# Kernel optimization log

Measured on AMD Instinct MI355X. Metric: run time of the kernel, lower is better.

## Reference

```python
import jax, jax.numpy as jnp
import numpy as np
import math

BATCH, NODES, IN_DIM = 8, 2048, 64
HEADS, OUT_DIM = 4, 32
D = HEADS * OUT_DIM
N_NEIGHBORS = 32


def setup_inputs() -> dict:
    key = jax.random.key(0)
    ks = jax.random.split(key, 6)
    s = lambda fan: 1.0 / np.sqrt(fan)
    return {
        "x": jax.random.normal(ks[0], (BATCH, NODES, IN_DIM), jnp.float32),
        "Wq": jax.random.normal(ks[1], (D, IN_DIM), jnp.float32) * s(IN_DIM),
        "bq": jnp.zeros((D,), jnp.float32),
        "Wk": jax.random.normal(ks[2], (D, IN_DIM), jnp.float32) * s(IN_DIM),
        "bk": jnp.zeros((D,), jnp.float32),
        "mlp_w": jax.random.normal(ks[3], (HEADS, HEADS), jnp.float32) * s(HEADS),
        "mlp_b": jnp.zeros((HEADS,), jnp.float32),
        "ln_g": jnp.ones((NODES,), jnp.float32),
        "ln_b": jnp.zeros((NODES,), jnp.float32),
    }


def _layernorm(x, g, b, eps=1e-5):
    m = x.mean(-1, keepdims=True)
    v = x.var(-1, keepdims=True)
    return (x - m) * jax.lax.rsqrt(v + eps) * g + b


def _forward(x, Wq, bq, Wk, bk, mlp_w, mlp_b, ln_g, ln_b):
    B, N, _ = x.shape
    # static graph branch (computed in the original forward, but its result is
    # never used in the returned adjacency -- kept for fidelity; DCE'd under jit)
    adj_static = jax.nn.softmax(
        jax.nn.relu(_layernorm(jnp.einsum('bnc,bmc->bnm', x, x), ln_g, ln_b)), axis=1)
    del adj_static

    q = x @ Wq.T + bq  # (B,N,D)
    k = x @ Wk.T + bk
    # (B,D,N) -> (B,H,d,N)
    q = q.transpose(0, 2, 1).reshape(B, HEADS, OUT_DIM, N)
    k = k.transpose(0, 2, 1).reshape(B, HEADS, OUT_DIM, N)
    q = q.transpose(0, 1, 3, 2)  # (B,H,N,d)

    # torch.split(query, chunk, dim=-1) splits q over out_dim, k over nodes; zip
    # truncates to the shorter list -> only min(nq,nk) chunks are processed.
    chunk = math.ceil(N / 2)
    nq = math.ceil(OUT_DIM / chunk)
    nk = math.ceil(N / chunk)
    inv_sqrt_d = jnp.float32(1.0 / math.sqrt(OUT_DIM))
    outs = []
    for i in range(min(nq, nk)):
        qc = q[..., i * chunk:(i + 1) * chunk]          # (B,H,N,dc)
        kc = k[..., i * chunk:(i + 1) * chunk]          # (B,H,d,Uc)
        a = jnp.einsum('bhnd,bhdu->bhnu', qc, kc) * inv_sqrt_d
        # dropout is identity in eval mode; soft-threshold with beta=0
        a = jnp.sign(a) * jax.nn.relu(jnp.abs(a))
        # 1x1 conv over head channels + relu, residual add
        a = jax.nn.relu(jnp.einsum('oh,bhnu->bonu', mlp_w, a)
                        + mlp_b[None, :, None, None]) + a
        outs.append(a)
    attn = jnp.concatenate(outs, axis=-1)               # (B,H,N,U)

    scores = attn.sum(axis=1)                           # (B,N,U)
    vals, idx = jax.lax.top_k(scores, N_NEIGHBORS)      # sorted, largest
    adj = jnp.zeros((B, N, N), x.dtype)
    bi = jnp.arange(B)[:, None, None]
    ni = jnp.arange(N)[None, :, None]
    return adj.at[bi, ni, idx].add(vals)


def reference(x, Wq, bq, Wk, bk, mlp_w, mlp_b, ln_g, ln_b):
    return _forward(x, Wq, bq, Wk, bk, mlp_w, mlp_b, ln_g, ln_b)
```

## Files before the change

kernel.cpp:

```cpp
#include <hip/hip_runtime.h>
#include <cstdint>
#include <cstddef>

#define BATCH 8
#define NODES 2048
#define IN_DIM 64
#define DTOT 128
#define NKEY 1024
#define QGROUPS 128
#define KGROUPS 64
#define SROW 1028

typedef _Float16 half8v __attribute__((ext_vector_type(8)));
typedef float float4v __attribute__((ext_vector_type(4)));
typedef float float2v __attribute__((ext_vector_type(2)));

__device__ __forceinline__ unsigned long long make_key(float v, int idx) {
    unsigned u = __float_as_uint(v);
    u = (u & 0x80000000u) ? ~u : (u | 0x80000000u);
    return ((unsigned long long)u << 32) | (unsigned)(1023 - idx);
}

__device__ __forceinline__ float key_val(unsigned hi) {
    return __uint_as_float((hi & 0x80000000u) ? (hi & 0x7fffffffu) : ~hi);
}

__global__ __launch_bounds__(256) void proj_qk(
    const float* __restrict__ x, const float* __restrict__ Wq, const float* __restrict__ bq,
    const float* __restrict__ Wk, const float* __restrict__ bk,
    _Float16* __restrict__ qfh, _Float16* __restrict__ qfl,
    _Float16* __restrict__ kfh, _Float16* __restrict__ kfl)
{
    __shared__ float xs[64 * 68];
    __shared__ float wsh[64 * 68];

    const int t = threadIdx.x;
    const int blk = blockIdx.x;
    const int b = blk / 96;
    const int idx = blk - b * 96;

    const float* W; const float* bias;
    _Float16* oh; _Float16* ol;
    int nbase, cbase; size_t gbase;
    float scale;
    if (idx < 64) {
        int nt = idx >> 1, ct = idx & 1;
        nbase = nt * 64; cbase = ct * 64;
        W = Wq; bias = bq; oh = qfh; ol = qfl;
        gbase = (size_t)b * QGROUPS + (nbase >> 4);
        scale = 0.17677669529663687f;
    } else {
        int i2 = idx - 64;
        int nt = i2 >> 1, ct = i2 & 1;
        nbase = nt * 64; cbase = ct * 64;
        W = Wk; bias = bk; oh = kfh; ol = kfl;
        gbase = (size_t)b * KGROUPS + (nbase >> 4);
        scale = 1.0f;
    }
    const int hbase = cbase >> 5;

    #pragma unroll
    for (int rep = 0; rep < 4; ++rep) {
        int f = rep * 256 + t;
        int r = f >> 4, d4 = f & 15;
        float4 xv = *(const float4*)(x + ((size_t)(b * NODES + nbase + r)) * IN_DIM + d4 * 4);
        *(float4*)(xs + r * 68 + d4 * 4) = xv;
        float4 wv = *(const float4*)(W + (size_t)(cbase + r) * IN_DIM + d4 * 4);
        *(float4*)(wsh + r * 68 + d4 * 4) = wv;
    }
    __syncthreads();

    const int w = t >> 6, l = t & 63;
    const int n_sel = w * 4 + (l >> 4);
    const int ul = l & 15;

    float acc[4][4];
    #pragma unroll
    for (int i = 0; i < 4; ++i)
        #pragma unroll
        for (int j = 0; j < 4; ++j) acc[i][j] = 0.f;

    #pragma unroll
    for (int d4 = 0; d4 < 16; ++d4) {
        float4 xv[4], wv[4];
        #pragma unroll
        for (int i = 0; i < 4; ++i)
            xv[i] = *(const float4*)(xs + (n_sel * 4 + i) * 68 + d4 * 4);
        #pragma unroll
        for (int j = 0; j < 4; ++j)
            wv[j] = *(const float4*)(wsh + (j * 16 + ul) * 68 + d4 * 4);
        #pragma unroll
        for (int i = 0; i < 4; ++i)
            #pragma unroll
            for (int j = 0; j < 4; ++j)
                acc[i][j] += xv[i].x * wv[j].x + xv[i].y * wv[j].y +
                             xv[i].z * wv[j].z + xv[i].w * wv[j].w;
    }
    __syncthreads();

    #pragma unroll
    for (int j = 0; j < 4; ++j) {
        float bv = bias[cbase + j * 16 + ul];
        #pragma unroll
        for (int i = 0; i < 4; ++i)
            xs[(n_sel * 4 + i) * 68 + j * 16 + ul] = (acc[i][j] + bv) * scale;
    }
    __syncthreads();

    #pragma unroll
    for (int rep = 0; rep < 2; ++rep) {
        int u = rep * 256 + t;
        int g = u >> 7, hh = (u >> 6) & 1, lf = u & 63;
        const float* src = xs + (g * 16 + (lf & 15)) * 68 + hh * 32 + (lf >> 4) * 8;
        float4 f0 = *(const float4*)src;
        float4 f1 = *(const float4*)(src + 4);
        float tmp[8] = {f0.x, f0.y, f0.z, f0.w, f1.x, f1.y, f1.z, f1.w};
        half8v hv, lv;
        #pragma unroll
        for (int e = 0; e < 8; ++e) {
            _Float16 hi = (_Float16)tmp[e];
            hv[e] = hi;
            lv[e] = (_Float16)(tmp[e] - (float)hi);
        }
        size_t dst = ((gbase + g) * 4 + hbase + hh) * (size_t)512 + lf * 8;
        *(half8v*)(oh + dst) = hv;
        *(half8v*)(ol + dst) = lv;
    }
}

__global__ __launch_bounds__(512, 4) void scores_topk(
    const _Float16* __restrict__ qfh, const _Float16* __restrict__ qfl,
    const _Float16* __restrict__ kfh, const _Float16* __restrict__ kfl,
    const float* __restrict__ mlpw, const float* __restrict__ mlpb,
    float* __restrict__ adj)
{
    __shared__ float sc[16 * SROW];
    __shared__ unsigned long long cand[8][64];

    const int t = threadIdx.x;
    const int blk = blockIdx.x;
    const int b = blk & 7;
    const int gq = blk >> 3;

    const int w = t >> 6, l = t & 63;
    const int quad = l >> 4, lane16 = l & 15;

    half8v Ah[4], Al[4];
    #pragma unroll
    for (int h = 0; h < 4; ++h) {
        size_t a = (((size_t)b * QGROUPS + gq) * 4 + h) * 512 + l * 8;
        Ah[h] = *(const half8v*)(qfh + a);
        Al[h] = *(const half8v*)(qfl + a);
    }

    float2v mw2[4][4], mb2[4];
    #pragma unroll
    for (int o = 0; o < 4; ++o) {
        float bvo = mlpb[o];
        mb2[o] = (float2v){bvo, bvo};
        #pragma unroll
        for (int h = 0; h < 4; ++h) {
            float mwo = mlpw[o * 4 + h];
            mw2[o][h] = (float2v){mwo, mwo};
        }
    }
    const float2v z2 = {0.f, 0.f};

    half8v Bh[4], Bl[4];
    {
        size_t a0 = (((size_t)b * KGROUPS + w * 8) * 4) * (size_t)512 + l * 8;
        #pragma unroll
        for (int h = 0; h < 4; ++h) {
            Bh[h] = *(const half8v*)(kfh + a0 + h * 512);
            Bl[h] = *(const half8v*)(kfl + a0 + h * 512);
        }
    }

    #pragma unroll
    for (int i = 0; i < 8; ++i) {
        const int g = w * 8 + i;
        half8v Bhn[4], Bln[4];
        if (i < 7) {
            size_t a1 = (((size_t)b * KGROUPS + g + 1) * 4) * (size_t)512 + l * 8;
            #pragma unroll
            for (int h = 0; h < 4; ++h) {
                Bhn[h] = *(const half8v*)(kfh + a1 + h * 512);
                Bln[h] = *(const half8v*)(kfl + a1 + h * 512);
            }
        }

        float4v C[4];
        #pragma unroll
        for (int h = 0; h < 4; ++h) {
            float4v c = {0.f, 0.f, 0.f, 0.f};
            c = __builtin_amdgcn_mfma_f32_16x16x32_f16(Ah[h], Bh[h], c, 0, 0, 0);
            c = __builtin_amdgcn_mfma_f32_16x16x32_f16(Ah[h], Bl[h], c, 0, 0, 0);
            c = __builtin_amdgcn_mfma_f32_16x16x32_f16(Al[h], Bh[h], c, 0, 0, 0);
            C[h] = c;
        }

        #pragma unroll
        for (int r2 = 0; r2 < 2; ++r2) {
            float2v a0 = {C[0][2 * r2], C[0][2 * r2 + 1]};
            float2v a1 = {C[1][2 * r2], C[1][2 * r2 + 1]};
            float2v a2 = {C[2][2 * r2], C[2][2 * r2 + 1]};
            float2v a3 = {C[3][2 * r2], C[3][2 * r2 + 1]};
            float2v ssum = ((a0 + a1) + a2) + a3;
            #pragma unroll
            for (int o = 0; o < 4; ++o) {
                float2v to = a0 * mw2[o][0] + a1 * mw2[o][1] +
                             a2 * mw2[o][2] + a3 * mw2[o][3] + mb2[o];
                ssum += __builtin_elementwise_max(to, z2);
            }
            const int col = g * 16 + lane16;
            sc[(quad * 4 + 2 * r2) * SROW + col] = ssum[0];
            sc[(quad * 4 + 2 * r2 + 1) * SROW + col] = ssum[1];
        }

        if (i < 7) {
            #pragma unroll
            for (int h = 0; h < 4; ++h) { Bh[h] = Bhn[h]; Bl[h] = Bln[h]; }
        }
    }
    __syncthreads();

    for (int rr = 0; rr < 2; ++rr) {
        const int row = w * 2 + rr;
        float* R = sc + row * SROW;

        float4 vv[4];
        #pragma unroll
        for (int jj = 0; jj < 4; ++jj) vv[jj] = *(const float4*)(R + jj * 256 + l * 4);

        float m = vv[0].x;
        #pragma unroll
        for (int jj = 0; jj < 4; ++jj) {
            m = fmaxf(m, vv[jj].x); m = fmaxf(m, vv[jj].y);
            m = fmaxf(m, vv[jj].z); m = fmaxf(m, vv[jj].w);
        }

        unsigned km;
        { unsigned s = __float_as_uint(m); km = (s & 0x80000000u) ? ~s : (s | 0x80000000u); }
        unsigned accT = 0u;
        #pragma unroll
        for (int bit = 31; bit >= 0; --bit) {
            unsigned trial = accT | (1u << bit);
            if (__popcll(__ballot(km >= trial)) >= 32) accT = trial;
        }
        const float T = key_val(accT);

        cand[w][l] = 0ull;
        __builtin_amdgcn_wave_barrier();
        int total = 0;
        #pragma unroll
        for (int jj = 0; jj < 4; ++jj) {
            #pragma unroll
            for (int e = 0; e < 4; ++e) {
                float v = (e == 0) ? vv[jj].x : (e == 1) ? vv[jj].y : (e == 2) ? vv[jj].z : vv[jj].w;
                bool p = (v >= T);
                unsigned long long msk = __ballot(p);
                if (p) {
                    int pos = total + __popcll(msk & ((1ull << l) - 1ull));
                    if (pos < 64) cand[w][pos] = make_key(v, jj * 256 + l * 4 + e);
                }
                total += (int)__popcll(msk);
            }
        }
        __builtin_amdgcn_wave_barrier();

        bool win = false; float wval = 0.f; int widx = 0;
        if (total <= 64) {
            unsigned long long key = cand[w][l];
            unsigned hi = (unsigned)(key >> 32), lo = (unsigned)key;

            unsigned X = 0u;
            #pragma unroll
            for (int bit = 31; bit >= 0; --bit) {
                unsigned trial = X | (1u << bit);
                if (__popcll(__ballot(hi >= trial)) >= 32) X = trial;
            }
            int cgt = __popcll(__ballot(hi > X));
            int rem = 32 - cgt;
            unsigned Y = 0u;
            #pragma unroll
            for (int bit = 9; bit >= 0; --bit) {
                unsigned trial = Y | (1u << bit);
                if (__popcll(__ballot(hi == X && lo >= trial)) >= rem) Y = trial;
            }
            if (hi > X || (hi == X && lo >= Y)) {
                win = true;
                wval = key_val(hi);
                widx = 1023 - (int)lo;
            }
        } else {
            float vals[16];
            #pragma unroll
            for (int jj = 0; jj < 4; ++jj) {
                vals[jj * 4 + 0] = vv[jj].x; vals[jj * 4 + 1] = vv[jj].y;
                vals[jj * 4 + 2] = vv[jj].z; vals[jj * 4 + 3] = vv[jj].w;
            }
            float selv = 0.f; int seli = 0;
            #pragma unroll 1
            for (int it = 0; it < 32; ++it) {
                float bv = -3.4e38f; int bi = 0x7fffffff;
                #pragma unroll
                for (int s = 0; s < 16; ++s) {
                    int idx2 = (s >> 2) * 256 + l * 4 + (s & 3);
                    if (vals[s] > bv) { bv = vals[s]; bi = idx2; }
                }
                #pragma unroll
                for (int off = 1; off < 64; off <<= 1) {
                    float ov = __shfl_xor(bv, off, 64);
                    int oi = __shfl_xor(bi, off, 64);
                    if (ov > bv || (ov == bv && oi < bi)) { bv = ov; bi = oi; }
                }
                if (l == it) { selv = bv; seli = bi; }
                if (((bi >> 2) & 63) == l) {
                    int slot = ((bi >> 8) << 2) + (bi & 3);
                    #pragma unroll
                    for (int s = 0; s < 16; ++s) if (s == slot) vals[s] = -3.4e38f;
                }
            }
            if (l < 32) { win = true; wval = selv; widx = seli; }
        }

        __builtin_amdgcn_wave_barrier();
        #pragma unroll
        for (int jj = 0; jj < 4; ++jj)
            *(float4*)(R + jj * 256 + l * 4) = make_float4(0.f, 0.f, 0.f, 0.f);
        __builtin_amdgcn_wave_barrier();
        if (win) R[widx] = wval;
        __builtin_amdgcn_wave_barrier();

        float* rowptr = adj + ((size_t)(b * NODES + gq * 16 + row)) * NODES;
        #pragma unroll
        for (int jj = 0; jj < 8; ++jj) {
            int c4 = jj * 64 + l;
            float4 val;
            if (c4 < 256) val = *(const float4*)(R + c4 * 4);
            else          val = make_float4(0.f, 0.f, 0.f, 0.f);
            *(float4*)(rowptr + c4 * 4) = val;
        }
    }
}

extern "C" void kernel_launch(void* const* d_in, const int* in_sizes, int n_in,
                              void* d_out, int out_size, void* d_ws, size_t ws_size,
                              hipStream_t stream) {
    const float* x    = (const float*)d_in[0];
    const float* Wq   = (const float*)d_in[1];
    const float* bq   = (const float*)d_in[2];
    const float* Wk   = (const float*)d_in[3];
    const float* bk   = (const float*)d_in[4];
    const float* mlpw = (const float*)d_in[5];
    const float* mlpb = (const float*)d_in[6];

    _Float16* qfh = (_Float16*)d_ws;
    _Float16* qfl = qfh + (size_t)BATCH * NODES * DTOT;
    _Float16* kfh = qfl + (size_t)BATCH * NODES * DTOT;
    _Float16* kfl = kfh + (size_t)BATCH * NKEY * DTOT;
    float* adj = (float*)d_out;

    proj_qk<<<dim3(BATCH * 96), dim3(256), 0, stream>>>(x, Wq, bq, Wk, bk, qfh, qfl, kfh, kfl);
    scores_topk<<<dim3(BATCH * QGROUPS), dim3(512), 0, stream>>>(qfh, qfl, kfh, kfl, mlpw, mlpb, adj);
}
```

Measured before the change: 184.5 us.

## Fuse Q projection into scores kernel and shorten top-k threshold search

```diff
diff --git a/kernel.cpp b/kernel.cpp
--- a/kernel.cpp
+++ b/kernel.cpp
@@ -25,10 +25,8 @@
     return __uint_as_float((hi & 0x80000000u) ? (hi & 0x7fffffffu) : ~hi);
 }
 
-__global__ __launch_bounds__(256) void proj_qk(
-    const float* __restrict__ x, const float* __restrict__ Wq, const float* __restrict__ bq,
-    const float* __restrict__ Wk, const float* __restrict__ bk,
-    _Float16* __restrict__ qfh, _Float16* __restrict__ qfl,
+__global__ __launch_bounds__(256) void proj_k(
+    const float* __restrict__ x, const float* __restrict__ Wk, const float* __restrict__ bk,
     _Float16* __restrict__ kfh, _Float16* __restrict__ kfl)
 {
     __shared__ float xs[64 * 68];
@@ -36,27 +34,11 @@
 
     const int t = threadIdx.x;
     const int blk = blockIdx.x;
-    const int b = blk / 96;
-    const int idx = blk - b * 96;
-
-    const float* W; const float* bias;
-    _Float16* oh; _Float16* ol;
-    int nbase, cbase; size_t gbase;
-    float scale;
-    if (idx < 64) {
-        int nt = idx >> 1, ct = idx & 1;
-        nbase = nt * 64; cbase = ct * 64;
-        W = Wq; bias = bq; oh = qfh; ol = qfl;
-        gbase = (size_t)b * QGROUPS + (nbase >> 4);
-        scale = 0.17677669529663687f;
-    } else {
-        int i2 = idx - 64;
-        int nt = i2 >> 1, ct = i2 & 1;
-        nbase = nt * 64; cbase = ct * 64;
-        W = Wk; bias = bk; oh = kfh; ol = kfl;
-        gbase = (size_t)b * KGROUPS + (nbase >> 4);
-        scale = 1.0f;
-    }
+    const int b = blk >> 5;
+    const int idx = blk & 31;
+    const int nbase = (idx >> 1) * 64;
+    const int cbase = (idx & 1) * 64;
+    const size_t gbase = (size_t)b * KGROUPS + (nbase >> 4);
     const int hbase = cbase >> 5;
 
     #pragma unroll
@@ -65,7 +47,7 @@
         int r = f >> 4, d4 = f & 15;
         float4 xv = *(const float4*)(x + ((size_t)(b * NODES + nbase + r)) * IN_DIM + d4 * 4);
         *(float4*)(xs + r * 68 + d4 * 4) = xv;
-        float4 wv = *(const float4*)(W + (size_t)(cbase + r) * IN_DIM + d4 * 4);
+        float4 wv = *(const float4*)(Wk + (size_t)(cbase + r) * IN_DIM + d4 * 4);
         *(float4*)(wsh + r * 68 + d4 * 4) = wv;
     }
     __syncthreads();
@@ -100,10 +82,10 @@
 
     #pragma unroll
     for (int j = 0; j < 4; ++j) {
-        float bv = bias[cbase + j * 16 + ul];
+        float bv = bk[cbase + j * 16 + ul];
         #pragma unroll
         for (int i = 0; i < 4; ++i)
-            xs[(n_sel * 4 + i) * 68 + j * 16 + ul] = (acc[i][j] + bv) * scale;
+            xs[(n_sel * 4 + i) * 68 + j * 16 + ul] = acc[i][j] + bv;
     }
     __syncthreads();
 
@@ -123,13 +105,13 @@
             lv[e] = (_Float16)(tmp[e] - (float)hi);
         }
         size_t dst = ((gbase + g) * 4 + hbase + hh) * (size_t)512 + lf * 8;
-        *(half8v*)(oh + dst) = hv;
-        *(half8v*)(ol + dst) = lv;
+        *(half8v*)(kfh + dst) = hv;
+        *(half8v*)(kfl + dst) = lv;
     }
 }
 
 __global__ __launch_bounds__(512, 4) void scores_topk(
-    const _Float16* __restrict__ qfh, const _Float16* __restrict__ qfl,
+    const float* __restrict__ x, const float* __restrict__ Wq, const float* __restrict__ bq,
     const _Float16* __restrict__ kfh, const _Float16* __restrict__ kfl,
     const float* __restrict__ mlpw, const float* __restrict__ mlpb,
     float* __restrict__ adj)
@@ -145,13 +127,52 @@
     const int w = t >> 6, l = t & 63;
     const int quad = l >> 4, lane16 = l & 15;
 
+    float* xq = sc;
+    float* qt = sc + 16 * 68;
+
+    if (t < 256) {
+        int r = t >> 4, d4 = t & 15;
+        float4 v = *(const float4*)(x + ((size_t)(b * NODES + gq * 16 + r)) * IN_DIM + d4 * 4);
+        *(float4*)(xq + r * 68 + d4 * 4) = v;
+    }
+    __syncthreads();
+
+    {
+        const int c = t & 127, rg = t >> 7;
+        const float INVS = 0.17677669529663687f;
+        float bv = bq[c];
+        float acc[4] = {bv, bv, bv, bv};
+        #pragma unroll
+        for (int d4 = 0; d4 < 16; ++d4) {
+            float4 w4 = *(const float4*)(Wq + (size_t)c * IN_DIM + d4 * 4);
+            #pragma unroll
+            for (int i = 0; i < 4; ++i) {
+                float4 x4 = *(const float4*)(xq + (rg * 4 + i) * 68 + d4 * 4);
+                acc[i] += w4.x * x4.x + w4.y * x4.y + w4.z * x4.z + w4.w * x4.w;
+            }
+        }
+        __syncthreads();
+        #pragma unroll
+        for (int i = 0; i < 4; ++i)
+            qt[(rg * 4 + i) * 132 + c] = acc[i] * INVS;
+    }
+    __syncthreads();
+
     half8v Ah[4], Al[4];
     #pragma unroll
     for (int h = 0; h < 4; ++h) {
-        size_t a = (((size_t)b * QGROUPS + gq) * 4 + h) * 512 + l * 8;
-        Ah[h] = *(const half8v*)(qfh + a);
-        Al[h] = *(const half8v*)(qfl + a);
-    }
+        const float* qp = qt + lane16 * 132 + h * 32 + quad * 8;
+        float4 f0 = *(const float4*)qp;
+        float4 f1 = *(const float4*)(qp + 4);
+        float tmp[8] = {f0.x, f0.y, f0.z, f0.w, f1.x, f1.y, f1.z, f1.w};
+        #pragma unroll
+        for (int e = 0; e < 8; ++e) {
+            _Float16 hi = (_Float16)tmp[e];
+            Ah[h][e] = hi;
+            Al[h][e] = (_Float16)(tmp[e] - (float)hi);
+        }
+    }
+    __syncthreads();
 
     float2v mw2[4][4], mb2[4];
     #pragma unroll
@@ -243,7 +264,7 @@
         { unsigned s = __float_as_uint(m); km = (s & 0x80000000u) ? ~s : (s | 0x80000000u); }
         unsigned accT = 0u;
         #pragma unroll
-        for (int bit = 31; bit >= 0; --bit) {
+        for (int bit = 31; bit >= 16; --bit) {
             unsigned trial = accT | (1u << bit);
             if (__popcll(__ballot(km >= trial)) >= 32) accT = trial;
         }
@@ -355,12 +376,10 @@
     const float* mlpw = (const float*)d_in[5];
     const float* mlpb = (const float*)d_in[6];
 
-    _Float16* qfh = (_Float16*)d_ws;
-    _Float16* qfl = qfh + (size_t)BATCH * NODES * DTOT;
-    _Float16* kfh = qfl + (size_t)BATCH * NODES * DTOT;
+    _Float16* kfh = (_Float16*)d_ws;
     _Float16* kfl = kfh + (size_t)BATCH * NKEY * DTOT;
     float* adj = (float*)d_out;
 
-    proj_qk<<<dim3(BATCH * 96), dim3(256), 0, stream>>>(x, Wq, bq, Wk, bk, qfh, qfl, kfh, kfl);
-    scores_topk<<<dim3(BATCH * QGROUPS), dim3(512), 0, stream>>>(qfh, qfl, kfh, kfl, mlpw, mlpb, adj);
-}
+    proj_k<<<dim3(BATCH * 32), dim3(256), 0, stream>>>(x, Wk, bk, kfh, kfl);
+    scores_topk<<<dim3(BATCH * QGROUPS), dim3(512), 0, stream>>>(x, Wq, bq, kfh, kfl, mlpw, mlpb, adj);
+}
```

Result: slower. 188.4 us (+2.1%).
